# Kernel tuning notes

Measured on AMD Instinct MI355X. Metric: run time of the kernel, lower is better.

The kernel has to match this reference:

```python
import jax, jax.numpy as jnp
import numpy as np


def setup_inputs() -> dict:
    key = jax.random.key(0)
    kx, ke = jax.random.split(key)
    B, D, H, W, K = 64, 64, 32, 32, 512
    x = jax.random.normal(kx, (B, D, H, W), dtype=jnp.float32)
    # matches nn.init.normal_(weight, mean=0.0, std=2*D**-0.5)
    emb = jax.random.normal(ke, (D, K), dtype=jnp.float32) * (2.0 * D ** -0.5)
    return {"x": x, "emb": emb}


def reference(x, emb):
    # x: (B, D, *spatial), emb: (D, K)
    B, D = x.shape[0], x.shape[1]
    spatial = x.shape[2:]
    xf = jnp.moveaxis(x, 1, -1).reshape(B, -1, D)  # (B, N, D)
    scores = -2.0 * jnp.einsum('bnd,dk->bnk', xf, emb) + jnp.sum(emb * emb, axis=0)  # (B, N, K)
    argmin = jnp.argmin(scores, axis=-1)  # (B, N) int
    quant = jnp.take(emb.T, argmin, axis=0)  # (B, N, D) gather from codebook
    result = jnp.moveaxis(quant.reshape(B, *spatial, D), -1, 1)  # (B, D, *spatial)
    return result, argmin.reshape(B, *spatial)
```

## Files before the change

kernel.cpp:

```cpp
#include <hip/hip_runtime.h>


constexpr int D   = 64;
constexpr int K   = 512;
constexpr int HW  = 1024;
constexpr int RPW = 16;

__global__ __launch_bounds__(256, 4) void vq_argmin_kernel(
    const float* __restrict__ x,
    const float* __restrict__ emb,
    float* __restrict__ out_q,
    float* __restrict__ out_idx)
{
    const int tid  = threadIdx.x;
    const int lane = tid & 63;
    const int wv   = __builtin_amdgcn_readfirstlane(tid >> 6);
    const int r0   = blockIdx.x * 64 + wv * RPW;
    const int b    = r0 >> 10;
    const int n0   = r0 & 1023;

    const float* xb = x + (size_t)b * D * HW + n0;

    float best[RPW];
    int   bidx[RPW];
    #pragma unroll
    for (int r = 0; r < RPW; ++r) { best[r] = 3.4e38f; bidx[r] = 0; }

    for (int cs = 0; cs < 8; ++cs) {
        const int kc = cs * 64 + lane;
        const float* ecol = emb + kc;

        float acc[RPW];
        #pragma unroll
        for (int r = 0; r < RPW; ++r) acc[r] = 0.f;
        float acc2 = 0.f;

        for (int dt = 0; dt < 4; ++dt) {
            #pragma unroll
            for (int dd = 0; dd < 16; ++dd) {
                const int d = dt * 16 + dd;
                const float ev = ecol[(size_t)d * K];
                acc2 = fmaf(ev, ev, acc2);
                const float* xp = xb + (size_t)d * HW;
                #pragma unroll
                for (int r = 0; r < RPW; ++r)
                    acc[r] = fmaf(ev, xp[r], acc[r]);
            }
        }

        #pragma unroll
        for (int r = 0; r < RPW; ++r) {
            float s = fmaf(-2.f, acc[r], acc2);
            if (s < best[r]) { best[r] = s; bidx[r] = kc; }
        }
    }

    #pragma unroll
    for (int r = 0; r < RPW; ++r) {
        float bs = best[r]; int bi = bidx[r];
        #pragma unroll
        for (int off = 32; off >= 1; off >>= 1) {
            float os = __shfl_xor(bs, off);
            int   oi = __shfl_xor(bi, off);
            if (os < bs || (os == bs && oi < bi)) { bs = os; bi = oi; }
        }
        best[r] = bs; bidx[r] = bi;
    }

    const int rr = lane & 15;
    int kq = bidx[0];
    #pragma unroll
    for (int r = 1; r < RPW; ++r) kq = (rr == r) ? bidx[r] : kq;

    if (lane < RPW)
        __builtin_nontemporal_store((float)kq, &out_idx[r0 + lane]);

    const int dsub = lane >> 4;
    float* oqb = out_q + (size_t)b * D * HW + n0 + rr;
    #pragma unroll 4
    for (int dt = 0; dt < 16; ++dt) {
        const int d = dt * 4 + dsub;
        __builtin_nontemporal_store(emb[(size_t)d * K + kq],
                                    &oqb[(size_t)d * HW]);
    }
}

extern "C" void kernel_launch(void* const* d_in, const int* in_sizes, int n_in,
                              void* d_out, int out_size, void* d_ws, size_t ws_size,
                              hipStream_t stream)
{
    const float* x   = (const float*)d_in[0];
    const float* emb = (const float*)d_in[1];

    float* out_q   = (float*)d_out;
    float* out_idx = out_q + (size_t)64 * 64 * 1024;

    vq_argmin_kernel<<<1024, 256, 0, stream>>>(x, emb, out_q, out_idx);
}
```

Baseline: 144.9 us.

## Precompute transposed codebook with norms and split codewords across waves

A small prologue kernel transposes the codebook into a workspace in record layout, one 68-float record per code holding its 64 components and its squared norm. The main kernel now has each pair of waves split the 512 codes, merges the per-row minima through LDS, and doubles the grid to 2048 blocks. The goal is more parallelism and occupancy, dropping the per-code norm recomputation, and vectorised f4 loads of code vectors. In exchange it adds a second launch and an LDS merge with two barriers. Its per-lane strided record loads are less coalesced than the old lane-contiguous column reads.

```diff
diff --git a/kernel.cpp b/kernel.cpp
--- a/kernel.cpp
+++ b/kernel.cpp
@@ -4,59 +4,85 @@
 constexpr int D   = 64;
 constexpr int K   = 512;
 constexpr int HW  = 1024;
-constexpr int RPW = 16;
+constexpr int REC = 68;
 
-__global__ __launch_bounds__(256, 4) void vq_argmin_kernel(
+typedef float f4 __attribute__((ext_vector_type(4)));
+
+__global__ __launch_bounds__(256) void emb_transpose_kernel(
+    const float* __restrict__ emb, float* __restrict__ ws)
+{
+    const int k = blockIdx.x * 256 + threadIdx.x;
+    if (k < K) {
+        float s = 0.f;
+        #pragma unroll 16
+        for (int d = 0; d < D; ++d) {
+            float v = emb[d * K + k];
+            ws[k * REC + d] = v;
+            s = fmaf(v, v, s);
+        }
+        ws[k * REC + 64] = s;
+    }
+}
+
+__global__ __launch_bounds__(256, 6) void vq_argmin_kernel(
     const float* __restrict__ x,
-    const float* __restrict__ emb,
+    const float* __restrict__ ws,
     float* __restrict__ out_q,
     float* __restrict__ out_idx)
 {
+    __shared__ float mbs[2][32];
+    __shared__ int   mis[2][32];
+    __shared__ int   kfin[32];
+
     const int tid  = threadIdx.x;
     const int lane = tid & 63;
     const int wv   = __builtin_amdgcn_readfirstlane(tid >> 6);
-    const int r0   = blockIdx.x * 64 + wv * RPW;
+    const int wrow = wv & 1;
+    const int wcs  = wv >> 1;
+    const int r0   = blockIdx.x * 32 + wrow * 16;
     const int b    = r0 >> 10;
     const int n0   = r0 & 1023;
 
     const float* xb = x + (size_t)b * D * HW + n0;
 
-    float best[RPW];
-    int   bidx[RPW];
+    float best[16];
+    int   bidx[16];
     #pragma unroll
-    for (int r = 0; r < RPW; ++r) { best[r] = 3.4e38f; bidx[r] = 0; }
+    for (int r = 0; r < 16; ++r) { best[r] = 3.4e38f; bidx[r] = 0; }
 
-    for (int cs = 0; cs < 8; ++cs) {
-        const int kc = cs * 64 + lane;
-        const float* ecol = emb + kc;
+    for (int cs = 0; cs < 4; ++cs) {
+        const int kc = (wcs * 4 + cs) * 64 + lane;
+        const float* cb = ws + kc * REC;
 
-        float acc[RPW];
+        float acc[16];
         #pragma unroll
-        for (int r = 0; r < RPW; ++r) acc[r] = 0.f;
-        float acc2 = 0.f;
+        for (int r = 0; r < 16; ++r) acc[r] = 0.f;
 
-        for (int dt = 0; dt < 4; ++dt) {
+        f4 evc = *(const f4*)cb;
+        for (int dt = 0; dt < 16; ++dt) {
+            f4 evn = *(const f4*)(cb + (dt + 1) * 4);
             #pragma unroll
-            for (int dd = 0; dd < 16; ++dd) {
-                const int d = dt * 16 + dd;
-                const float ev = ecol[(size_t)d * K];
-                acc2 = fmaf(ev, ev, acc2);
+            for (int j = 0; j < 4; ++j) {
+                const int d = dt * 4 + j;
+                const float ev = evc[j];
                 const float* xp = xb + (size_t)d * HW;
                 #pragma unroll
-                for (int r = 0; r < RPW; ++r)
+                for (int r = 0; r < 16; ++r)
                     acc[r] = fmaf(ev, xp[r], acc[r]);
             }
+            evc = evn;
         }
 
+        const float e2 = cb[64];
         #pragma unroll
-        for (int r = 0; r < RPW; ++r) {
-            float s = fmaf(-2.f, acc[r], acc2);
+        for (int r = 0; r < 16; ++r) {
+            float s = fmaf(-2.f, acc[r], e2);
             if (s < best[r]) { best[r] = s; bidx[r] = kc; }
         }
     }
 
     #pragma unroll
-    for (int r = 0; r < RPW; ++r) {
+    for (int r = 0; r < 16; ++r) {
         float bs = best[r]; int bi = bidx[r];
         #pragma unroll
         for (int off = 32; off >= 1; off >>= 1) {
@@ -68,20 +94,34 @@
     }
 
     const int rr = lane & 15;
-    int kq = bidx[0];
+    float bs = best[0]; int bi = bidx[0];
     #pragma unroll
-    for (int r = 1; r < RPW; ++r) kq = (rr == r) ? bidx[r] : kq;
+    for (int r = 1; r < 16; ++r)
+        if (rr == r) { bs = best[r]; bi = bidx[r]; }
 
-    if (lane < RPW)
-        __builtin_nontemporal_store((float)kq, &out_idx[r0 + lane]);
+    if (lane < 16) { mbs[wcs][wrow * 16 + lane] = bs; mis[wcs][wrow * 16 + lane] = bi; }
+    __syncthreads();
 
-    const int dsub = lane >> 4;
-    float* oqb = out_q + (size_t)b * D * HW + n0 + rr;
-    #pragma unroll 4
-    for (int dt = 0; dt < 16; ++dt) {
-        const int d = dt * 4 + dsub;
-        __builtin_nontemporal_store(emb[(size_t)d * K + kq],
-                                    &oqb[(size_t)d * HW]);
+    const int rb0 = blockIdx.x * 32;
+    if (tid < 32) {
+        float b0 = mbs[0][tid]; int i0 = mis[0][tid];
+        float b1 = mbs[1][tid]; int i1 = mis[1][tid];
+        int kq = (b1 < b0) ? i1 : i0;
+        kfin[tid] = kq;
+        __builtin_nontemporal_store((float)kq, &out_idx[rb0 + tid]);
+    }
+    __syncthreads();
+
+    const int bb  = rb0 >> 10;
+    const int nn0 = rb0 & 1023;
+    const int row   = tid & 31;
+    const int dslot = tid >> 5;
+    const float* cq = ws + kfin[row] * REC;
+    float* oqb = out_q + (size_t)bb * D * HW + nn0 + row;
+    #pragma unroll
+    for (int jj = 0; jj < 8; ++jj) {
+        const int d = jj * 8 + dslot;
+        __builtin_nontemporal_store(cq[d], &oqb[(size_t)d * HW]);
     }
 }
 
@@ -94,6 +134,9 @@
 
     float* out_q   = (float*)d_out;
     float* out_idx = out_q + (size_t)64 * 64 * 1024;
+    float* ws      = (float*)d_ws;
 
-    vq_argmin_kernel<<<1024, 256, 0, stream>>>(x, emb, out_q, out_idx);
+    emb_transpose_kernel<<<2, 256, 0, stream>>>(emb, ws);
+
+    vq_argmin_kernel<<<2048, 256, 0, stream>>>(x, ws, out_q, out_idx);
 }
```

Result: slower. 160.2 us (+10.6%).
